# Optimization experiments

Hardware: AMD Instinct MI355X
Metric: run time of the kernel (lower is better)

## Reference

```python
import jax, jax.numpy as jnp
import numpy as np

B, D, H = 131072, 8, 128


def setup_inputs() -> dict:
    key = jax.random.key(0)
    ks = jax.random.split(key, 8)
    s1 = 1.0 / np.sqrt(D + 1)
    s2 = 1.0 / np.sqrt(H)
    return {
        "z": jax.random.normal(ks[0], (B, D), dtype=jnp.float32),
        "logp_z": jnp.zeros((B, 1), dtype=jnp.float32),
        "t": jax.random.uniform(ks[1], (1,), dtype=jnp.float32),
        "W1": jax.random.normal(ks[2], (D + 1, H), dtype=jnp.float32) * s1,
        "b1": jnp.zeros((H,), dtype=jnp.float32),
        "W2": jax.random.normal(ks[3], (H, H), dtype=jnp.float32) * s2,
        "b2": jnp.zeros((H,), dtype=jnp.float32),
        "W3": jax.random.normal(ks[4], (H, D), dtype=jnp.float32) * s2,
        "b3": jnp.zeros((D,), dtype=jnp.float32),
    }


def _net_single(z_i, t_scalar, W1, b1, W2, b2, W3, b3):
    # z_i: [D] -> dz/dt: [D]; FFJORD-style MLP on concat([z, t])
    x = jnp.concatenate([z_i, t_scalar[None]])  # [D+1]
    h = jnp.tanh(x @ W1 + b1)
    h = jnp.tanh(h @ W2 + b2)
    return h @ W3 + b3


def reference(z, logp_z, t, W1, b1, W2, b2, W3, b3):
    t_scalar = t.reshape(())

    def f_i(z_i):
        return _net_single(z_i, t_scalar, W1, b1, W2, b2, W3, b3)

    # dz/dt for every sample (batched forward)
    dz_dt = jax.vmap(f_i)(z)  # [B, D]
    # Exact Jacobian trace: fused forward-mode batched Jacobian (replaces the
    # original's D sequential autograd.grad reverse-mode calls)
    jac = jax.vmap(jax.jacfwd(f_i))(z)  # [B, D, D]
    trace = jnp.einsum("bii->b", jac)  # [B]
    dlogp_z_dt = -trace[:, None]  # [B, 1]
    return (dz_dt, dlogp_z_dt)
```

## Files before the change

kernel.cpp:

```cpp
#include <hip/hip_runtime.h>
#include <hip/hip_bf16.h>

#define BATCH 131072
#define PITCH_H 72

typedef __bf16 bf16x8 __attribute__((ext_vector_type(8)));
typedef float floatx4 __attribute__((ext_vector_type(4)));

__device__ __forceinline__ float fast_tanh(float x) {
    float e = __expf(2.0f * x);
    return 1.0f - 2.0f * __builtin_amdgcn_rcpf(e + 1.0f);
}


__global__ void prep_kernel(const float* __restrict__ W1,
                            const float* __restrict__ W2,
                            const float* __restrict__ W3,
                            __bf16* __restrict__ ws) {
    int idx = blockIdx.x * 256 + threadIdx.x;
    if (idx < 16384) {
        int j = idx & 7, q = (idx >> 3) & 3, n = (idx >> 5) & 127, kb = idx >> 12;
        int k = kb * 32 + q * 8 + j;
        ws[idx] = (__bf16)W2[k * 128 + n];
        float c = 0.0f;
        #pragma unroll
        for (int d = 0; d < 8; ++d) c += W3[k * 8 + d] * W1[d * 128 + n];
        ws[16384 + idx] = (__bf16)(W2[n * 128 + k] * c);
    } else if (idx < 20480) {
        int t = idx - 16384;
        int j = t & 7, q = (t >> 3) & 3, n = t >> 5;
        int k = q * 8 + j;
        ws[32768 + t] = (k < 9) ? (__bf16)W1[k * 128 + n] : (__bf16)0.0f;
    } else if (idx < 22528) {
        int t = idx - 20480;
        int j = t & 7, q = (t >> 3) & 3, n = (t >> 5) & 15, kb = t >> 9;
        int k = kb * 32 + q * 8 + j;
        ws[36864 + t] = (n < 8) ? (__bf16)W3[k * 8 + n] : (__bf16)0.0f;
    }
}

__global__ __launch_bounds__(256, 2) void cnf_main(
        const float* __restrict__ z, const float* __restrict__ t_ptr,
        const float* __restrict__ b1g, const float* __restrict__ b2g,
        const float* __restrict__ b3g, const __bf16* __restrict__ ws,
        float* __restrict__ out) {
    __shared__ __bf16 sW2s[16384];
    __shared__ __bf16 sGTs[16384];
    __shared__ float sb1[128];
    __shared__ float sb2[128];
    __shared__ __bf16 tile[4][16 * PITCH_H];

    const int tid = threadIdx.x;
    {
        uint4* dst = (uint4*)sW2s;
        const uint4* src = (const uint4*)ws;
        #pragma unroll
        for (int i = 0; i < 8; ++i) dst[tid + i * 256] = src[tid + i * 256];
        uint4* dstg = (uint4*)sGTs;
        const uint4* srcg = (const uint4*)(ws + 16384);
        #pragma unroll
        for (int i = 0; i < 8; ++i) dstg[tid + i * 256] = srcg[tid + i * 256];
        if (tid < 128) { sb1[tid] = b1g[tid]; sb2[tid] = b2g[tid]; }
    }
    __syncthreads();

    const int lane = tid & 63;
    const int w = tid >> 6;
    const int p = lane & 15;
    const int q = lane >> 4;
    __bf16* T = tile[w];
    const float tval = t_ptr[0];
    const float b3v = (p < 8) ? b3g[p] : 0.0f;
    const bf16x8* W2sv = (const bf16x8*)sW2s;
    const bf16x8* GTsv = (const bf16x8*)sGTs;
    const bf16x8* W1g  = (const bf16x8*)(ws + 32768);
    const bf16x8* W3g  = (const bf16x8*)(ws + 36864);

    bf16x8 w1f[8];
    #pragma unroll
    for (int nt = 0; nt < 8; ++nt) w1f[nt] = W1g[(nt * 16 + p) * 4 + q];
    bf16x8 w3f[4];
    #pragma unroll
    for (int kb = 0; kb < 4; ++kb) w3f[kb] = W3g[(kb * 16 + p) * 4 + q];

    #pragma unroll
    for (int it = 0; it < 2; ++it) {
        const int s0 = blockIdx.x * 128 + it * 64 + w * 16;

        bf16x8 ax;
        #pragma unroll
        for (int j = 0; j < 8; ++j) ax[j] = (__bf16)0.0f;
        if (q == 0) {
            const float4 z0 = ((const float4*)(z + (size_t)(s0 + p) * 8))[0];
            const float4 z1 = ((const float4*)(z + (size_t)(s0 + p) * 8))[1];
            ax[0] = (__bf16)z0.x; ax[1] = (__bf16)z0.y;
            ax[2] = (__bf16)z0.z; ax[3] = (__bf16)z0.w;
            ax[4] = (__bf16)z1.x; ax[5] = (__bf16)z1.y;
            ax[6] = (__bf16)z1.z; ax[7] = (__bf16)z1.w;
        } else if (q == 1) {
            ax[0] = (__bf16)tval;
        }

        float a1c[32];
        bf16x8 ah[4];
        #pragma unroll
        for (int half = 0; half < 2; ++half) {
            #pragma unroll
            for (int nt = half * 4; nt < half * 4 + 4; ++nt) {
                const int n = nt * 16 + p;
                floatx4 acc = {0.f, 0.f, 0.f, 0.f};
                acc = __builtin_amdgcn_mfma_f32_16x16x32_bf16(ax, w1f[nt], acc, 0, 0, 0);
                const float bn = sb1[n];
                #pragma unroll
                for (int r = 0; r < 4; ++r) {
                    const float h1 = fast_tanh(acc[r] + bn);
                    a1c[nt * 4 + r] = __builtin_fmaf(-h1, h1, 1.0f);
                    T[(q * 4 + r) * PITCH_H + (nt - half * 4) * 16 + p] = (__bf16)h1;
                }
            }
            ah[half * 2 + 0] = *(const bf16x8*)&T[p * PITCH_H + q * 8];
            ah[half * 2 + 1] = *(const bf16x8*)&T[p * PITCH_H + 32 + q * 8];
        }

        bf16x8 ah2[4];
        #pragma unroll
        for (int half = 0; half < 2; ++half) {
            #pragma unroll
            for (int nt = half * 4; nt < half * 4 + 4; ++nt) {
                const int n = nt * 16 + p;
                floatx4 acc = {0.f, 0.f, 0.f, 0.f};
                #pragma unroll
                for (int kb = 0; kb < 4; ++kb)
                    acc = __builtin_amdgcn_mfma_f32_16x16x32_bf16(
                            ah[kb], W2sv[(kb * 128 + n) * 4 + q], acc, 0, 0, 0);
                const float bn = sb2[n];
                #pragma unroll
                for (int r = 0; r < 4; ++r) {
                    const float h2 = fast_tanh(acc[r] + bn);
                    T[(q * 4 + r) * PITCH_H + (nt - half * 4) * 16 + p] = (__bf16)h2;
                }
            }
            ah2[half * 2 + 0] = *(const bf16x8*)&T[p * PITCH_H + q * 8];
            ah2[half * 2 + 1] = *(const bf16x8*)&T[p * PITCH_H + 32 + q * 8];
        }

        bf16x8 aa[4];
        #pragma unroll
        for (int kb = 0; kb < 4; ++kb) {
            #pragma unroll
            for (int j = 0; j < 8; ++j) {
                const float f = (float)ah2[kb][j];
                aa[kb][j] = (__bf16)__builtin_fmaf(-f, f, 1.0f);
            }
        }

        floatx4 acc3 = {0.f, 0.f, 0.f, 0.f};
        #pragma unroll
        for (int kb = 0; kb < 4; ++kb)
            acc3 = __builtin_amdgcn_mfma_f32_16x16x32_bf16(
                    ah2[kb], w3f[kb], acc3, 0, 0, 0);
        if (p < 8) {
            #pragma unroll
            for (int r = 0; r < 4; ++r)
                out[(size_t)(s0 + q * 4 + r) * 8 + p] = acc3[r] + b3v;
        }

        float tr[4] = {0.f, 0.f, 0.f, 0.f};
        #pragma unroll
        for (int nt = 0; nt < 8; ++nt) {
            const int n = nt * 16 + p;
            floatx4 acc = {0.f, 0.f, 0.f, 0.f};
            #pragma unroll
            for (int kb = 0; kb < 4; ++kb)
                acc = __builtin_amdgcn_mfma_f32_16x16x32_bf16(
                        aa[kb], GTsv[(kb * 128 + n) * 4 + q], acc, 0, 0, 0);
            #pragma unroll
            for (int r = 0; r < 4; ++r)
                tr[r] = __builtin_fmaf(a1c[nt * 4 + r], acc[r], tr[r]);
        }

        #pragma unroll
        for (int r = 0; r < 4; ++r) {
            float v = tr[r];
            v += __shfl_xor(v, 1, 64);
            v += __shfl_xor(v, 2, 64);
            v += __shfl_xor(v, 4, 64);
            v += __shfl_xor(v, 8, 64);
            tr[r] = v;
        }
        if (p == 0) {
            #pragma unroll
            for (int r = 0; r < 4; ++r)
                out[(size_t)BATCH * 8 + s0 + q * 4 + r] = -tr[r];
        }
    }
}

extern "C" void kernel_launch(void* const* d_in, const int* in_sizes, int n_in,
                              void* d_out, int out_size, void* d_ws, size_t ws_size,
                              hipStream_t stream) {
    const float* z  = (const float*)d_in[0];
    const float* t  = (const float*)d_in[2];
    const float* W1 = (const float*)d_in[3];
    const float* b1 = (const float*)d_in[4];
    const float* W2 = (const float*)d_in[5];
    const float* b2 = (const float*)d_in[6];
    const float* W3 = (const float*)d_in[7];
    const float* b3 = (const float*)d_in[8];
    __bf16* ws = (__bf16*)d_ws;
    float* out = (float*)d_out;

    prep_kernel<<<88, 256, 0, stream>>>(W1, W2, W3, ws);
    cnf_main<<<1024, 256, 0, stream>>>(z, t, b1, b2, b3, ws, out);
}
```

Measured before the change: 96.31 us.

## Interleave two sample tiles per wave and issue global loads before LDS staging

```diff
diff --git a/kernel.cpp b/kernel.cpp
--- a/kernel.cpp
+++ b/kernel.cpp
@@ -39,6 +39,111 @@
     }
 }
 
+
+__device__ __forceinline__ void phase0_h1(
+        const bf16x8& ax, const bf16x8* w1f, const float* sb1,
+        __bf16* T, int p, int q, float* a1c, bf16x8* ah) {
+    #pragma unroll
+    for (int half = 0; half < 2; ++half) {
+        #pragma unroll
+        for (int lt = 0; lt < 4; ++lt) {
+            const int nt = half * 4 + lt;
+            const int n = nt * 16 + p;
+            floatx4 acc = {0.f, 0.f, 0.f, 0.f};
+            acc = __builtin_amdgcn_mfma_f32_16x16x32_bf16(ax, w1f[nt], acc, 0, 0, 0);
+            const float bn = sb1[n];
+            #pragma unroll
+            for (int r = 0; r < 4; ++r) {
+                const float h1 = fast_tanh(acc[r] + bn);
+                a1c[nt * 4 + r] = __builtin_fmaf(-h1, h1, 1.0f);
+                T[(q * 4 + r) * PITCH_H + lt * 16 + p] = (__bf16)h1;
+            }
+        }
+        ah[half * 2 + 0] = *(const bf16x8*)&T[p * PITCH_H + q * 8];
+        ah[half * 2 + 1] = *(const bf16x8*)&T[p * PITCH_H + 32 + q * 8];
+    }
+}
+
+__device__ __forceinline__ void phase1_h2(
+        const bf16x8* ah, const bf16x8* W2sv, const float* sb2,
+        __bf16* T, int p, int q, bf16x8* ah2, bf16x8* aa) {
+    #pragma unroll
+    for (int half = 0; half < 2; ++half) {
+        #pragma unroll
+        for (int lt = 0; lt < 4; ++lt) {
+            const int nt = half * 4 + lt;
+            const int n = nt * 16 + p;
+            floatx4 acc = {0.f, 0.f, 0.f, 0.f};
+            #pragma unroll
+            for (int kb = 0; kb < 4; ++kb)
+                acc = __builtin_amdgcn_mfma_f32_16x16x32_bf16(
+                        ah[kb], W2sv[(kb * 128 + n) * 4 + q], acc, 0, 0, 0);
+            const float bn = sb2[n];
+            #pragma unroll
+            for (int r = 0; r < 4; ++r) {
+                const float h2 = fast_tanh(acc[r] + bn);
+                T[(q * 4 + r) * PITCH_H + lt * 16 + p] = (__bf16)h2;
+            }
+        }
+        ah2[half * 2 + 0] = *(const bf16x8*)&T[p * PITCH_H + q * 8];
+        ah2[half * 2 + 1] = *(const bf16x8*)&T[p * PITCH_H + 32 + q * 8];
+    }
+    #pragma unroll
+    for (int kb = 0; kb < 4; ++kb) {
+        #pragma unroll
+        for (int j = 0; j < 8; ++j) {
+            const float f = (float)ah2[kb][j];
+            aa[kb][j] = (__bf16)__builtin_fmaf(-f, f, 1.0f);
+        }
+    }
+}
+
+__device__ __forceinline__ void phase3_dz(
+        const bf16x8* ah2, const bf16x8* w3f, float b3v,
+        int s0, int p, int q, float* out) {
+    floatx4 acc3 = {0.f, 0.f, 0.f, 0.f};
+    #pragma unroll
+    for (int kb = 0; kb < 4; ++kb)
+        acc3 = __builtin_amdgcn_mfma_f32_16x16x32_bf16(ah2[kb], w3f[kb], acc3, 0, 0, 0);
+    if (p < 8) {
+        #pragma unroll
+        for (int r = 0; r < 4; ++r)
+            out[(size_t)(s0 + q * 4 + r) * 8 + p] = acc3[r] + b3v;
+    }
+}
+
+__device__ __forceinline__ void phase2_tr(
+        const bf16x8* aa, const float* a1c, const bf16x8* GTsv,
+        int s0, int p, int q, float* out) {
+    float tr[4] = {0.f, 0.f, 0.f, 0.f};
+    #pragma unroll
+    for (int nt = 0; nt < 8; ++nt) {
+        const int n = nt * 16 + p;
+        floatx4 acc = {0.f, 0.f, 0.f, 0.f};
+        #pragma unroll
+        for (int kb = 0; kb < 4; ++kb)
+            acc = __builtin_amdgcn_mfma_f32_16x16x32_bf16(
+                    aa[kb], GTsv[(kb * 128 + n) * 4 + q], acc, 0, 0, 0);
+        #pragma unroll
+        for (int r = 0; r < 4; ++r)
+            tr[r] = __builtin_fmaf(a1c[nt * 4 + r], acc[r], tr[r]);
+    }
+    #pragma unroll
+    for (int r = 0; r < 4; ++r) {
+        float v = tr[r];
+        v += __shfl_xor(v, 1, 64);
+        v += __shfl_xor(v, 2, 64);
+        v += __shfl_xor(v, 4, 64);
+        v += __shfl_xor(v, 8, 64);
+        tr[r] = v;
+    }
+    if (p == 0) {
+        #pragma unroll
+        for (int r = 0; r < 4; ++r)
+            out[(size_t)BATCH * 8 + s0 + q * 4 + r] = -tr[r];
+    }
+}
+
 __global__ __launch_bounds__(256, 2) void cnf_main(
         const float* __restrict__ z, const float* __restrict__ t_ptr,
         const float* __restrict__ b1g, const float* __restrict__ b2g,
@@ -51,149 +156,77 @@
     __shared__ __bf16 tile[4][16 * PITCH_H];
 
     const int tid = threadIdx.x;
-    {
-        uint4* dst = (uint4*)sW2s;
-        const uint4* src = (const uint4*)ws;
-        #pragma unroll
-        for (int i = 0; i < 8; ++i) dst[tid + i * 256] = src[tid + i * 256];
-        uint4* dstg = (uint4*)sGTs;
-        const uint4* srcg = (const uint4*)(ws + 16384);
-        #pragma unroll
-        for (int i = 0; i < 8; ++i) dstg[tid + i * 256] = srcg[tid + i * 256];
-        if (tid < 128) { sb1[tid] = b1g[tid]; sb2[tid] = b2g[tid]; }
-    }
-    __syncthreads();
-
     const int lane = tid & 63;
     const int w = tid >> 6;
     const int p = lane & 15;
     const int q = lane >> 4;
+    const int sbase = blockIdx.x * 128 + w * 32;
+    const float tval = t_ptr[0];
+
+    bf16x8 ax0, ax1;
+    #pragma unroll
+    for (int j = 0; j < 8; ++j) { ax0[j] = (__bf16)0.0f; ax1[j] = (__bf16)0.0f; }
+    if (q == 0) {
+        const float4* zp0 = (const float4*)(z + (size_t)(sbase + p) * 8);
+        const float4* zp1 = (const float4*)(z + (size_t)(sbase + 16 + p) * 8);
+        const float4 a0 = zp0[0], a1 = zp0[1], c0 = zp1[0], c1 = zp1[1];
+        ax0[0] = (__bf16)a0.x; ax0[1] = (__bf16)a0.y;
+        ax0[2] = (__bf16)a0.z; ax0[3] = (__bf16)a0.w;
+        ax0[4] = (__bf16)a1.x; ax0[5] = (__bf16)a1.y;
+        ax0[6] = (__bf16)a1.z; ax0[7] = (__bf16)a1.w;
+        ax1[0] = (__bf16)c0.x; ax1[1] = (__bf16)c0.y;
+        ax1[2] = (__bf16)c0.z; ax1[3] = (__bf16)c0.w;
+        ax1[4] = (__bf16)c1.x; ax1[5] = (__bf16)c1.y;
+        ax1[6] = (__bf16)c1.z; ax1[7] = (__bf16)c1.w;
+    } else if (q == 1) {
+        ax0[0] = (__bf16)tval;
+        ax1[0] = (__bf16)tval;
+    }
+
+    const bf16x8* W1g = (const bf16x8*)(ws + 32768);
+    const bf16x8* W3g = (const bf16x8*)(ws + 36864);
+    bf16x8 w1f[8];
+    #pragma unroll
+    for (int nt = 0; nt < 8; ++nt) w1f[nt] = W1g[(nt * 16 + p) * 4 + q];
+    bf16x8 w3f[4];
+    #pragma unroll
+    for (int kb = 0; kb < 4; ++kb) w3f[kb] = W3g[(kb * 16 + p) * 4 + q];
+
+    {
+        uint4* dst = (uint4*)sW2s;
+        const uint4* src = (const uint4*)ws;
+        #pragma unroll
+        for (int i = 0; i < 8; ++i) dst[tid + i * 256] = src[tid + i * 256];
+        uint4* dstg = (uint4*)sGTs;
+        const uint4* srcg = (const uint4*)(ws + 16384);
+        #pragma unroll
+        for (int i = 0; i < 8; ++i) dstg[tid + i * 256] = srcg[tid + i * 256];
+        if (tid < 128) { sb1[tid] = b1g[tid]; sb2[tid] = b2g[tid]; }
+    }
+    __syncthreads();
+
     __bf16* T = tile[w];
-    const float tval = t_ptr[0];
-    const float b3v = (p < 8) ? b3g[p] : 0.0f;
     const bf16x8* W2sv = (const bf16x8*)sW2s;
     const bf16x8* GTsv = (const bf16x8*)sGTs;
-    const bf16x8* W1g  = (const bf16x8*)(ws + 32768);
-    const bf16x8* W3g  = (const bf16x8*)(ws + 36864);
-
-    bf16x8 w1f[8];
-    #pragma unroll
-    for (int nt = 0; nt < 8; ++nt) w1f[nt] = W1g[(nt * 16 + p) * 4 + q];
-    bf16x8 w3f[4];
-    #pragma unroll
-    for (int kb = 0; kb < 4; ++kb) w3f[kb] = W3g[(kb * 16 + p) * 4 + q];
-
-    #pragma unroll
-    for (int it = 0; it < 2; ++it) {
-        const int s0 = blockIdx.x * 128 + it * 64 + w * 16;
-
-        bf16x8 ax;
-        #pragma unroll
-        for (int j = 0; j < 8; ++j) ax[j] = (__bf16)0.0f;
-        if (q == 0) {
-            const float4 z0 = ((const float4*)(z + (size_t)(s0 + p) * 8))[0];
-            const float4 z1 = ((const float4*)(z + (size_t)(s0 + p) * 8))[1];
-            ax[0] = (__bf16)z0.x; ax[1] = (__bf16)z0.y;
-            ax[2] = (__bf16)z0.z; ax[3] = (__bf16)z0.w;
-            ax[4] = (__bf16)z1.x; ax[5] = (__bf16)z1.y;
-            ax[6] = (__bf16)z1.z; ax[7] = (__bf16)z1.w;
-        } else if (q == 1) {
-            ax[0] = (__bf16)tval;
-        }
-
-        float a1c[32];
-        bf16x8 ah[4];
-        #pragma unroll
-        for (int half = 0; half < 2; ++half) {
-            #pragma unroll
-            for (int nt = half * 4; nt < half * 4 + 4; ++nt) {
-                const int n = nt * 16 + p;
-                floatx4 acc = {0.f, 0.f, 0.f, 0.f};
-                acc = __builtin_amdgcn_mfma_f32_16x16x32_bf16(ax, w1f[nt], acc, 0, 0, 0);
-                const float bn = sb1[n];
-                #pragma unroll
-                for (int r = 0; r < 4; ++r) {
-                    const float h1 = fast_tanh(acc[r] + bn);
-                    a1c[nt * 4 + r] = __builtin_fmaf(-h1, h1, 1.0f);
-                    T[(q * 4 + r) * PITCH_H + (nt - half * 4) * 16 + p] = (__bf16)h1;
-                }
-            }
-            ah[half * 2 + 0] = *(const bf16x8*)&T[p * PITCH_H + q * 8];
-            ah[half * 2 + 1] = *(const bf16x8*)&T[p * PITCH_H + 32 + q * 8];
-        }
-
-        bf16x8 ah2[4];
-        #pragma unroll
-        for (int half = 0; half < 2; ++half) {
-            #pragma unroll
-            for (int nt = half * 4; nt < half * 4 + 4; ++nt) {
-                const int n = nt * 16 + p;
-                floatx4 acc = {0.f, 0.f, 0.f, 0.f};
-                #pragma unroll
-                for (int kb = 0; kb < 4; ++kb)
-                    acc = __builtin_amdgcn_mfma_f32_16x16x32_bf16(
-                            ah[kb], W2sv[(kb * 128 + n) * 4 + q], acc, 0, 0, 0);
-                const float bn = sb2[n];
-                #pragma unroll
-                for (int r = 0; r < 4; ++r) {
-                    const float h2 = fast_tanh(acc[r] + bn);
-                    T[(q * 4 + r) * PITCH_H + (nt - half * 4) * 16 + p] = (__bf16)h2;
-                }
-            }
-            ah2[half * 2 + 0] = *(const bf16x8*)&T[p * PITCH_H + q * 8];
-            ah2[half * 2 + 1] = *(const bf16x8*)&T[p * PITCH_H + 32 + q * 8];
-        }
-
-        bf16x8 aa[4];
-        #pragma unroll
-        for (int kb = 0; kb < 4; ++kb) {
-            #pragma unroll
-            for (int j = 0; j < 8; ++j) {
-                const float f = (float)ah2[kb][j];
-                aa[kb][j] = (__bf16)__builtin_fmaf(-f, f, 1.0f);
-            }
-        }
-
-        floatx4 acc3 = {0.f, 0.f, 0.f, 0.f};
-        #pragma unroll
-        for (int kb = 0; kb < 4; ++kb)
-            acc3 = __builtin_amdgcn_mfma_f32_16x16x32_bf16(
-                    ah2[kb], w3f[kb], acc3, 0, 0, 0);
-        if (p < 8) {
-            #pragma unroll
-            for (int r = 0; r < 4; ++r)
-                out[(size_t)(s0 + q * 4 + r) * 8 + p] = acc3[r] + b3v;
-        }
-
-        float tr[4] = {0.f, 0.f, 0.f, 0.f};
-        #pragma unroll
-        for (int nt = 0; nt < 8; ++nt) {
-            const int n = nt * 16 + p;
-            floatx4 acc = {0.f, 0.f, 0.f, 0.f};
-            #pragma unroll
-            for (int kb = 0; kb < 4; ++kb)
-                acc = __builtin_amdgcn_mfma_f32_16x16x32_bf16(
-                        aa[kb], GTsv[(kb * 128 + n) * 4 + q], acc, 0, 0, 0);
-            #pragma unroll
-            for (int r = 0; r < 4; ++r)
-                tr[r] = __builtin_fmaf(a1c[nt * 4 + r], acc[r], tr[r]);
-        }
-
-        #pragma unroll
-        for (int r = 0; r < 4; ++r) {
-            float v = tr[r];
-            v += __shfl_xor(v, 1, 64);
-            v += __shfl_xor(v, 2, 64);
-            v += __shfl_xor(v, 4, 64);
-            v += __shfl_xor(v, 8, 64);
-            tr[r] = v;
-        }
-        if (p == 0) {
-            #pragma unroll
-            for (int r = 0; r < 4; ++r)
-                out[(size_t)BATCH * 8 + s0 + q * 4 + r] = -tr[r];
-        }
-    }
+    const float b3v = (p < 8) ? b3g[p] : 0.0f;
+    const int s0a = sbase;
+    const int s0b = sbase + 16;
+
+    float a1c0[32], a1c1[32];
+    bf16x8 ah0[4], ah1[4];
+    phase0_h1(ax0, w1f, sb1, T, p, q, a1c0, ah0);
+    phase0_h1(ax1, w1f, sb1, T, p, q, a1c1, ah1);
+
+    bf16x8 ah2_0[4], aa0[4];
+    phase1_h2(ah0, W2sv, sb2, T, p, q, ah2_0, aa0);
+    phase3_dz(ah2_0, w3f, b3v, s0a, p, q, out);
+
+    bf16x8 ah2_1[4], aa1[4];
+    phase1_h2(ah1, W2sv, sb2, T, p, q, ah2_1, aa1);
+    phase2_tr(aa0, a1c0, GTsv, s0a, p, q, out);
+
+    phase3_dz(ah2_1, w3f, b3v, s0b, p, q, out);
+    phase2_tr(aa1, a1c1, GTsv, s0b, p, q, out);
 }
 
 extern "C" void kernel_launch(void* const* d_in, const int* in_sizes, int n_in,
```

Measured after the change: 97.32 us. About the same (+1.0%).
